# Optimization experiments

Hardware: AMD Instinct MI355X
Metric: run time of the kernel (lower is better)

The kernel has to match this reference:

```python
import jax, jax.numpy as jnp
import numpy as np

B, H, W, C = 32, 512, 512, 3


def dct2_matrix(N):
    # Orthonormal DCT-II basis: D[k, n] = s_k * sqrt(2/N) * cos(pi*(2n+1)*k/(2N))
    n = np.arange(N)
    k = n[:, None]
    D = np.cos(np.pi * (2 * n[None, :] + 1) * k / (2.0 * N)) * np.sqrt(2.0 / N)
    D[0, :] *= 1.0 / np.sqrt(2.0)  # ortho scaling of DC row
    return jnp.asarray(D, dtype=jnp.float32)


def setup_inputs() -> dict:
    key = jax.random.key(0)
    x = jax.random.normal(key, (B, H, W, C), dtype=jnp.float32)
    return {"x": x}


def reference(x) -> jnp.ndarray:
    # 2D DCT-II (ortho) along height and width, channels untouched.
    Dh = dct2_matrix(x.shape[1])  # [H, H]
    Dw = dct2_matrix(x.shape[2])  # [W, W]
    y = jnp.einsum('kh,bhwc->bkwc', Dh, x)   # DCT over height
    y = jnp.einsum('lw,bkwc->bklc', Dw, y)   # DCT over width
    return y
```

## Files before the change

### kernel.cpp

```cpp
#include <hip/hip_runtime.h>
#include <stdint.h>


typedef __bf16 bf16_t;
typedef bf16_t bf16x8 __attribute__((ext_vector_type(8)));
typedef bf16_t bf16x4 __attribute__((ext_vector_type(4)));
typedef float  f32x4  __attribute__((ext_vector_type(4)));

__device__ __forceinline__ uint32_t f2bf(float f) {
    union { float f; uint32_t u; } v; v.f = f;
    uint32_t r = v.u + 0x7fffu + ((v.u >> 16) & 1u);
    return r >> 16;
}

__device__ __forceinline__ f32x4 mfma16(bf16x8 a, bf16x8 b, f32x4 c) {
    return __builtin_amdgcn_mfma_f32_16x16x32_bf16(a, b, c, 0, 0, 0);
}

__device__ __forceinline__ void load_lds16(const void* g, void* l) {
    __builtin_amdgcn_global_load_lds(
        (const __attribute__((address_space(1))) uint32_t*)g,
        (__attribute__((address_space(3))) uint32_t*)l, 16, 0, 0);
}

__global__ __launch_bounds__(256) void gen_dct(uint16_t* __restrict__ Dbf) {
    int idx = blockIdx.x * 256 + threadIdx.x;
    int k = idx >> 9, h = idx & 511;
    int phase = ((2 * h + 1) * k) & 2047;
    float ang = (float)phase * 3.0679615757712823e-3f;
    float s = (k == 0) ? 0.04419417382415922f : 0.0625f;
    Dbf[idx] = (uint16_t)f2bf(__cosf(ang) * s);
}

__global__ __launch_bounds__(256, 4) void pass_w(const float* __restrict__ x,
                                                 const uint16_t* __restrict__ Dbf,
                                                 uint16_t* __restrict__ Y1) {
    __shared__ __align__(16) uint16_t Ax[96 * 64];
    __shared__ __align__(16) uint16_t Bd[128 * 64];
    const int t = threadIdx.x, lane = t & 63, wv = t >> 6;
    const int quad = lane >> 4, l15 = lane & 15;
    const int lt = blockIdx.x;
    const int ht = blockIdx.y;
    const int b  = blockIdx.z;

    const int hl = t >> 3, wq = t & 7;
    const float* xrow = x + (size_t)b * 786432 + (size_t)(ht * 32 + hl) * 1536 + wq * 24;

    const uint16_t* srcD[4];
#pragma unroll
    for (int i = 0; i < 4; ++i) {
        int p = i * 256 + t, row = p >> 3, jj = (p & 7) ^ (row & 7);
        srcD[i] = Dbf + (size_t)(lt * 128 + row) * 512 + jj * 8;
    }

    float4 xr[6];
#pragma unroll
    for (int i = 0; i < 6; ++i) xr[i] = *(const float4*)(xrow + i * 4);

    f32x4 acc[6][2] = {};

    for (int kt = 0; kt < 8; ++kt) {
        __syncthreads();
#pragma unroll
        for (int i = 0; i < 4; ++i)
            load_lds16(srcD[i] + kt * 64, Bd + (i * 256 + t) * 8);
        {
            const float* xf = (const float*)xr;
            const int wsw = ((wq + (hl & 7)) & 7) * 8;
#pragma unroll
            for (int c = 0; c < 3; ++c) {
                bf16x8 hv;
#pragma unroll
                for (int u = 0; u < 8; ++u) hv[u] = (bf16_t)xf[c + 3 * u];
                *(bf16x8*)&Ax[(c * 32 + hl) * 64 + wsw] = hv;
            }
        }
        __syncthreads();
        if (kt < 7) {
#pragma unroll
            for (int i = 0; i < 6; ++i)
                xr[i] = *(const float4*)(xrow + (kt + 1) * 192 + i * 4);
        }
#pragma unroll
        for (int ks = 0; ks < 2; ++ks) {
            bf16x8 aq[6], bq[2];
#pragma unroll
            for (int tt = 0; tt < 6; ++tt) {
                int m = tt * 16 + l15;
                int ws = ((ks * 4 + quad + (m & 7)) & 7) * 8;
                aq[tt] = *(const bf16x8*)&Ax[m * 64 + ws];
            }
#pragma unroll
            for (int p = 0; p < 2; ++p) {
                int n = wv * 32 + p * 16 + l15;
                int pos = n * 8 + ((ks * 4 + quad) ^ (n & 7));
                bq[p] = *(const bf16x8*)&Bd[pos * 8];
            }
#pragma unroll
            for (int tt = 0; tt < 6; ++tt)
#pragma unroll
                for (int p = 0; p < 2; ++p)
                    acc[tt][p] = mfma16(aq[tt], bq[p], acc[tt][p]);
        }
    }

#pragma unroll
    for (int tt = 0; tt < 6; ++tt) {
        const int c = tt >> 1;
        const int hb = (tt & 1) * 16 + quad * 4;
#pragma unroll
        for (int p = 0; p < 2; ++p) {
            int n = wv * 32 + p * 16 + l15;
            bf16x4 pk;
#pragma unroll
            for (int r = 0; r < 4; ++r) pk[r] = (bf16_t)acc[tt][p][r];
            *(bf16x4*)&Y1[(size_t)b * 786432 + (size_t)c * 262144 +
                          (size_t)(lt * 128 + n) * 512 + ht * 32 + hb] = pk;
        }
    }
}

__global__ __launch_bounds__(256, 4) void pass_h(const uint16_t* __restrict__ Y1,
                                                 const uint16_t* __restrict__ Dbf,
                                                 float* __restrict__ out) {
    __shared__ __align__(16) char smem[28672];
    uint16_t* Ad = (uint16_t*)smem;
    uint16_t* By = (uint16_t*)(smem + 16384);
    float*    El = (float*)smem;
    const int t = threadIdx.x, lane = t & 63, wv = t >> 6;
    const int quad = lane >> 4, l15 = lane & 15;
    const int ktile = blockIdx.x;
    const int lt = blockIdx.y;
    const int b  = blockIdx.z;
    const int l0 = lt * 32;

    const uint16_t* srcA[4];
#pragma unroll
    for (int i = 0; i < 4; ++i) {
        int p = i * 256 + t, row = p >> 3, jj = (p & 7) ^ (row & 7);
        srcA[i] = Dbf + (size_t)(ktile * 128 + row) * 512 + jj * 8;
    }
    const uint16_t* srcB[3];
#pragma unroll
    for (int i = 0; i < 3; ++i) {
        int p = i * 256 + t, row = p >> 3, jj = (p & 7) ^ (row & 7);
        srcB[i] = Y1 + (size_t)b * 786432 + (size_t)(row >> 5) * 262144 +
                  (size_t)(l0 + (row & 31)) * 512 + jj * 8;
    }

    uint4 yr[3];
#pragma unroll
    for (int i = 0; i < 3; ++i) yr[i] = *(const uint4*)srcB[i];

    f32x4 acc[6][2] = {};

    for (int kt = 0; kt < 8; ++kt) {
        __syncthreads();
#pragma unroll
        for (int i = 0; i < 4; ++i)
            load_lds16(srcA[i] + kt * 64, Ad + (i * 256 + t) * 8);
#pragma unroll
        for (int i = 0; i < 3; ++i)
            *(uint4*)&By[(i * 256 + t) * 8] = yr[i];
        __syncthreads();
        if (kt < 7) {
#pragma unroll
            for (int i = 0; i < 3; ++i)
                yr[i] = *(const uint4*)(srcB[i] + (kt + 1) * 64);
        }
#pragma unroll
        for (int ks = 0; ks < 2; ++ks) {
            bf16x8 aq[2], bq[6];
#pragma unroll
            for (int p = 0; p < 2; ++p) {
                int m = wv * 32 + p * 16 + l15;
                int pos = m * 8 + ((ks * 4 + quad) ^ (m & 7));
                aq[p] = *(const bf16x8*)&Ad[pos * 8];
            }
#pragma unroll
            for (int tt = 0; tt < 6; ++tt) {
                int n = tt * 16 + l15;
                int pos = n * 8 + ((ks * 4 + quad) ^ (n & 7));
                bq[tt] = *(const bf16x8*)&By[pos * 8];
            }
#pragma unroll
            for (int tt = 0; tt < 6; ++tt)
#pragma unroll
                for (int p = 0; p < 2; ++p)
                    acc[tt][p] = mfma16(aq[p], bq[tt], acc[tt][p]);
        }
    }

    const int sub = t & 3, krow = t >> 2;
#pragma unroll
    for (int ph = 0; ph < 2; ++ph) {
        __syncthreads();
        if ((wv >> 1) == ph) {
#pragma unroll
            for (int p = 0; p < 2; ++p) {
                int idx2 = wv * 2 + p;
                int kb = (idx2 & 3) * 16 + quad * 4;
#pragma unroll
                for (int tt = 0; tt < 6; ++tt) {
                    int n = tt * 16 + l15;
                    int col = (n & 31) * 3 + (n >> 5);
#pragma unroll
                    for (int r = 0; r < 4; ++r)
                        El[(kb + r) * 100 + col] = acc[tt][p][r];
                }
            }
        }
        __syncthreads();
        float* dst = out + (size_t)b * 786432 +
                     (size_t)(ktile * 128 + ph * 64 + krow) * 1536 + lt * 96 + sub * 24;
        const float* srcE = El + krow * 100 + sub * 24;
#pragma unroll
        for (int i = 0; i < 6; ++i)
            *(float4*)(dst + i * 4) = *(const float4*)(srcE + i * 4);
    }
}

extern "C" void kernel_launch(void* const* d_in, const int* in_sizes, int n_in,
                              void* d_out, int out_size, void* d_ws, size_t ws_size,
                              hipStream_t stream) {
    (void)in_sizes; (void)n_in; (void)out_size; (void)ws_size;
    const float* x = (const float*)d_in[0];
    float* out = (float*)d_out;
    uint16_t* Dbf = (uint16_t*)d_ws;
    uint16_t* Y1  = (uint16_t*)d_ws + 512 * 512;

    gen_dct<<<1024, 256, 0, stream>>>(Dbf);
    dim3 g1(4, 16, 32);
    pass_w<<<g1, 256, 0, stream>>>(x, Dbf, Y1);
    dim3 g2(4, 16, 32);
    pass_h<<<g2, 256, 0, stream>>>(Y1, Dbf, out);
}
```

Baseline: 303.2 us.

## Load DCT fragments directly to registers, shrink LDS, remap block order

```diff
diff --git a/kernel.cpp b/kernel.cpp
--- a/kernel.cpp
+++ b/kernel.cpp
@@ -15,12 +15,6 @@
 
 __device__ __forceinline__ f32x4 mfma16(bf16x8 a, bf16x8 b, f32x4 c) {
     return __builtin_amdgcn_mfma_f32_16x16x32_bf16(a, b, c, 0, 0, 0);
-}
-
-__device__ __forceinline__ void load_lds16(const void* g, void* l) {
-    __builtin_amdgcn_global_load_lds(
-        (const __attribute__((address_space(1))) uint32_t*)g,
-        (__attribute__((address_space(3))) uint32_t*)l, 16, 0, 0);
 }
 
 __global__ __launch_bounds__(256) void gen_dct(uint16_t* __restrict__ Dbf) {
@@ -32,26 +26,25 @@
     Dbf[idx] = (uint16_t)f2bf(__cosf(ang) * s);
 }
 
-__global__ __launch_bounds__(256, 4) void pass_w(const float* __restrict__ x,
+__device__ __forceinline__ void decode_bid(int bid, int& member, int& g) {
+    int low3 = bid & 7, rest = bid >> 3;
+    member = rest & 3;
+    g = (rest >> 2) * 8 + low3;
+}
+
+__global__ __launch_bounds__(256, 8) void pass_w(const float* __restrict__ x,
                                                  const uint16_t* __restrict__ Dbf,
                                                  uint16_t* __restrict__ Y1) {
     __shared__ __align__(16) uint16_t Ax[96 * 64];
-    __shared__ __align__(16) uint16_t Bd[128 * 64];
     const int t = threadIdx.x, lane = t & 63, wv = t >> 6;
     const int quad = lane >> 4, l15 = lane & 15;
-    const int lt = blockIdx.x;
-    const int ht = blockIdx.y;
-    const int b  = blockIdx.z;
+    int lt, g;
+    decode_bid(blockIdx.x, lt, g);
+    const int ht = g & 15, b = g >> 4;
 
     const int hl = t >> 3, wq = t & 7;
     const float* xrow = x + (size_t)b * 786432 + (size_t)(ht * 32 + hl) * 1536 + wq * 24;
-
-    const uint16_t* srcD[4];
-#pragma unroll
-    for (int i = 0; i < 4; ++i) {
-        int p = i * 256 + t, row = p >> 3, jj = (p & 7) ^ (row & 7);
-        srcD[i] = Dbf + (size_t)(lt * 128 + row) * 512 + jj * 8;
-    }
+    const uint16_t* dptr = Dbf + (size_t)(lt * 128 + wv * 32 + l15) * 512 + quad * 8;
 
     float4 xr[6];
 #pragma unroll
@@ -61,9 +54,6 @@
 
     for (int kt = 0; kt < 8; ++kt) {
         __syncthreads();
-#pragma unroll
-        for (int i = 0; i < 4; ++i)
-            load_lds16(srcD[i] + kt * 64, Bd + (i * 256 + t) * 8);
         {
             const float* xf = (const float*)xr;
             const int wsw = ((wq + (hl & 7)) & 7) * 8;
@@ -76,6 +66,12 @@
             }
         }
         __syncthreads();
+        bf16x8 dq[2][2];
+#pragma unroll
+        for (int ks = 0; ks < 2; ++ks)
+#pragma unroll
+            for (int p = 0; p < 2; ++p)
+                dq[ks][p] = *(const bf16x8*)(dptr + (size_t)p * 8192 + kt * 64 + ks * 32);
         if (kt < 7) {
 #pragma unroll
             for (int i = 0; i < 6; ++i)
@@ -83,7 +79,7 @@
         }
 #pragma unroll
         for (int ks = 0; ks < 2; ++ks) {
-            bf16x8 aq[6], bq[2];
+            bf16x8 aq[6];
 #pragma unroll
             for (int tt = 0; tt < 6; ++tt) {
                 int m = tt * 16 + l15;
@@ -91,16 +87,10 @@
                 aq[tt] = *(const bf16x8*)&Ax[m * 64 + ws];
             }
 #pragma unroll
-            for (int p = 0; p < 2; ++p) {
-                int n = wv * 32 + p * 16 + l15;
-                int pos = n * 8 + ((ks * 4 + quad) ^ (n & 7));
-                bq[p] = *(const bf16x8*)&Bd[pos * 8];
-            }
-#pragma unroll
             for (int tt = 0; tt < 6; ++tt)
 #pragma unroll
                 for (int p = 0; p < 2; ++p)
-                    acc[tt][p] = mfma16(aq[tt], bq[p], acc[tt][p]);
+                    acc[tt][p] = mfma16(aq[tt], dq[ks][p], acc[tt][p]);
         }
     }
 
@@ -120,26 +110,19 @@
     }
 }
 
-__global__ __launch_bounds__(256, 4) void pass_h(const uint16_t* __restrict__ Y1,
+__global__ __launch_bounds__(256, 8) void pass_h(const uint16_t* __restrict__ Y1,
                                                  const uint16_t* __restrict__ Dbf,
                                                  float* __restrict__ out) {
-    __shared__ __align__(16) char smem[28672];
-    uint16_t* Ad = (uint16_t*)smem;
-    uint16_t* By = (uint16_t*)(smem + 16384);
+    __shared__ __align__(16) char smem[12800];
+    uint16_t* By = (uint16_t*)smem;
     float*    El = (float*)smem;
     const int t = threadIdx.x, lane = t & 63, wv = t >> 6;
     const int quad = lane >> 4, l15 = lane & 15;
-    const int ktile = blockIdx.x;
-    const int lt = blockIdx.y;
-    const int b  = blockIdx.z;
+    int ktile, g;
+    decode_bid(blockIdx.x, ktile, g);
+    const int lt = g & 15, b = g >> 4;
     const int l0 = lt * 32;
 
-    const uint16_t* srcA[4];
-#pragma unroll
-    for (int i = 0; i < 4; ++i) {
-        int p = i * 256 + t, row = p >> 3, jj = (p & 7) ^ (row & 7);
-        srcA[i] = Dbf + (size_t)(ktile * 128 + row) * 512 + jj * 8;
-    }
     const uint16_t* srcB[3];
 #pragma unroll
     for (int i = 0; i < 3; ++i) {
@@ -147,6 +130,7 @@
         srcB[i] = Y1 + (size_t)b * 786432 + (size_t)(row >> 5) * 262144 +
                   (size_t)(l0 + (row & 31)) * 512 + jj * 8;
     }
+    const uint16_t* dptr = Dbf + (size_t)(ktile * 128 + wv * 32 + l15) * 512 + quad * 8;
 
     uint4 yr[3];
 #pragma unroll
@@ -156,13 +140,16 @@
 
     for (int kt = 0; kt < 8; ++kt) {
         __syncthreads();
-#pragma unroll
-        for (int i = 0; i < 4; ++i)
-            load_lds16(srcA[i] + kt * 64, Ad + (i * 256 + t) * 8);
 #pragma unroll
         for (int i = 0; i < 3; ++i)
             *(uint4*)&By[(i * 256 + t) * 8] = yr[i];
         __syncthreads();
+        bf16x8 dq[2][2];
+#pragma unroll
+        for (int ks = 0; ks < 2; ++ks)
+#pragma unroll
+            for (int p = 0; p < 2; ++p)
+                dq[ks][p] = *(const bf16x8*)(dptr + (size_t)p * 8192 + kt * 64 + ks * 32);
         if (kt < 7) {
 #pragma unroll
             for (int i = 0; i < 3; ++i)
@@ -170,13 +157,7 @@
         }
 #pragma unroll
         for (int ks = 0; ks < 2; ++ks) {
-            bf16x8 aq[2], bq[6];
-#pragma unroll
-            for (int p = 0; p < 2; ++p) {
-                int m = wv * 32 + p * 16 + l15;
-                int pos = m * 8 + ((ks * 4 + quad) ^ (m & 7));
-                aq[p] = *(const bf16x8*)&Ad[pos * 8];
-            }
+            bf16x8 bq[6];
 #pragma unroll
             for (int tt = 0; tt < 6; ++tt) {
                 int n = tt * 16 + l15;
@@ -187,35 +168,32 @@
             for (int tt = 0; tt < 6; ++tt)
 #pragma unroll
                 for (int p = 0; p < 2; ++p)
-                    acc[tt][p] = mfma16(aq[p], bq[tt], acc[tt][p]);
-        }
-    }
-
-    const int sub = t & 3, krow = t >> 2;
-#pragma unroll
-    for (int ph = 0; ph < 2; ++ph) {
-        __syncthreads();
-        if ((wv >> 1) == ph) {
-#pragma unroll
-            for (int p = 0; p < 2; ++p) {
-                int idx2 = wv * 2 + p;
-                int kb = (idx2 & 3) * 16 + quad * 4;
+                    acc[tt][p] = mfma16(dq[ks][p], bq[tt], acc[tt][p]);
+        }
+    }
+
+    const int krow = t >> 3, sub = t & 7;
+#pragma unroll
+    for (int ph = 0; ph < 4; ++ph) {
+        __syncthreads();
+        if (wv == ph) {
+#pragma unroll
+            for (int p = 0; p < 2; ++p)
 #pragma unroll
                 for (int tt = 0; tt < 6; ++tt) {
                     int n = tt * 16 + l15;
                     int col = (n & 31) * 3 + (n >> 5);
 #pragma unroll
                     for (int r = 0; r < 4; ++r)
-                        El[(kb + r) * 100 + col] = acc[tt][p][r];
+                        El[(p * 16 + quad * 4 + r) * 100 + col] = acc[tt][p][r];
                 }
-            }
         }
         __syncthreads();
         float* dst = out + (size_t)b * 786432 +
-                     (size_t)(ktile * 128 + ph * 64 + krow) * 1536 + lt * 96 + sub * 24;
-        const float* srcE = El + krow * 100 + sub * 24;
-#pragma unroll
-        for (int i = 0; i < 6; ++i)
+                     (size_t)(ktile * 128 + ph * 32 + krow) * 1536 + lt * 96 + sub * 12;
+        const float* srcE = El + krow * 100 + sub * 12;
+#pragma unroll
+        for (int i = 0; i < 3; ++i)
             *(float4*)(dst + i * 4) = *(const float4*)(srcE + i * 4);
     }
 }
@@ -230,8 +208,6 @@
     uint16_t* Y1  = (uint16_t*)d_ws + 512 * 512;
 
     gen_dct<<<1024, 256, 0, stream>>>(Dbf);
-    dim3 g1(4, 16, 32);
-    pass_w<<<g1, 256, 0, stream>>>(x, Dbf, Y1);
-    dim3 g2(4, 16, 32);
-    pass_h<<<g2, 256, 0, stream>>>(Y1, Dbf, out);
-}
+    pass_w<<<2048, 256, 0, stream>>>(x, Dbf, Y1);
+    pass_h<<<2048, 256, 0, stream>>>(Y1, Dbf, out);
+}
```

Result: slower. 534.5 us (+76.3%).
